# Performance work log

Measured on AMD Instinct MI355X. Metric: run time of the kernel, lower is better.

## Reference

```python
import jax, jax.numpy as jnp
import numpy as np

B, L_MAX, D, RL, RD, DOUT = 64, 4096, 128, 64, 16, 512
LN_EPS = 1e-5

def _xavier(key, shape):
    fan_in, fan_out = shape[0], shape[1]
    limit = np.sqrt(6.0 / (fan_in + fan_out)).astype(np.float32)
    return jax.random.uniform(key, shape, jnp.float32, -limit, limit)

def setup_inputs() -> dict:
    key = jax.random.key(0)
    ks = jax.random.split(key, 10)
    emb = jax.random.normal(ks[0], (B, L_MAX, D), jnp.float32)
    # contiguous padding mask from random true lengths (standard ESM padding)
    lengths = jax.random.randint(ks[1], (B,), 1, L_MAX + 1)
    mask = (jnp.arange(L_MAX)[None, :] < lengths[:, None])  # bool [B, L_max]
    B_c = _xavier(ks[2], (D, RD))
    A_c = _xavier(ks[3], (L_MAX, RL))
    H_c = _xavier(ks[4], (RL * RD, DOUT))
    W1 = _xavier(ks[5], (DOUT, DOUT))
    b1 = jnp.zeros((DOUT,), jnp.float32)
    ln_w = jnp.ones((DOUT,), jnp.float32)
    ln_b = jnp.zeros((DOUT,), jnp.float32)
    W2 = _xavier(ks[6], (DOUT, DOUT))
    b2 = jnp.zeros((DOUT,), jnp.float32)
    return {"emb": emb, "mask": mask, "B_c": B_c, "A_c": A_c, "H_c": H_c,
            "W1": W1, "b1": b1, "ln_w": ln_w, "ln_b": ln_b, "W2": W2, "b2": b2}

def reference(emb, mask, B_c, A_c, H_c, W1, b1, ln_w, ln_b, W2, b2):
    m = mask.astype(emb.dtype)                      # [B, L]
    X = emb * m[:, :, None]                         # masked embeddings [B, L, D]
    Y = jnp.einsum('bld,dr->blr', X, B_c)           # low-rank proj over D -> [B, L, rD]
    U = jnp.einsum('blr,lk->bkr', Y, A_c)           # low-rank proj over L -> [B, rL, rD]
    z = U.reshape(U.shape[0], -1) @ H_c             # [B, d]
    # expander: Linear -> LayerNorm -> ReLU -> Linear
    h = z @ W1 + b1
    mu = jnp.mean(h, axis=-1, keepdims=True)
    var = jnp.mean(jnp.square(h - mu), axis=-1, keepdims=True)
    h = (h - mu) / jnp.sqrt(var + LN_EPS) * ln_w + ln_b
    h = jax.nn.relu(h)
    return h @ W2 + b2
```

## Files before the change

kernel.cpp:

```cpp
#include <hip/hip_runtime.h>


__global__ __launch_bounds__(256) void detect_mask(
    const unsigned int* __restrict__ m, int* __restrict__ flag)
{
    unsigned int v = 0;
    int base = (blockIdx.x * 256 + threadIdx.x) * 4;
#pragma unroll
    for (int i = 0; i < 4; ++i) v |= m[base + i];
    unsigned long long any = __ballot(v > 1u);
    if ((threadIdx.x & 63) == 0 && any) atomicOr(flag, 1);
}

#define BCS_CHUNK 516
__global__ __launch_bounds__(256, 3) void y_proj(
    const float* __restrict__ emb,
    const void* __restrict__ maskp,
    const float* __restrict__ Bc,
    float* __restrict__ Y,
    const int* __restrict__ flag)
{
    __shared__ __align__(16) float BcS[4 * BCS_CHUNK];

    const int tid = threadIdx.x;
    const int q   = tid & 3;
    const int r2  = tid >> 2;
    const int b   = blockIdx.x >> 5;
    const int rg  = blockIdx.x & 31;
    const long l0 = (long)rg * 128;
    const int byte_mode = *flag;

#pragma unroll
    for (int i = 0; i < 8; ++i) {
        int e = i * 256 + tid;
        int k = e >> 4, col = e & 15;
        BcS[(k >> 5) * BCS_CHUNK + (k & 31) * 16 + col] = Bc[e];
    }
    __syncthreads();

    const long row0 = (long)b * 4096 + l0 + r2;
    const long row1 = row0 + 64;
    const float* x0p = emb + row0 * 128 + q * 32;
    const float* x1p = emb + row1 * 128 + q * 32;
    float4 xv0[8], xv1[8];
#pragma unroll
    for (int j = 0; j < 8; ++j) xv0[j] = *(const float4*)(x0p + j * 4);
#pragma unroll
    for (int j = 0; j < 8; ++j) xv1[j] = *(const float4*)(x1p + j * 4);

    const float* bq = BcS + q * BCS_CHUNK;
    float y0[16], y1[16];
#pragma unroll
    for (int j = 0; j < 16; ++j) { y0[j] = 0.f; y1[j] = 0.f; }
#pragma unroll
    for (int j4 = 0; j4 < 8; ++j4) {
        float4 v0 = xv0[j4], v1 = xv1[j4];
#pragma unroll
        for (int i = 0; i < 4; ++i) {
            int kk = j4 * 4 + i;
            float xa = (i == 0) ? v0.x : (i == 1) ? v0.y : (i == 2) ? v0.z : v0.w;
            float xb = (i == 0) ? v1.x : (i == 1) ? v1.y : (i == 2) ? v1.z : v1.w;
#pragma unroll
            for (int c4 = 0; c4 < 4; ++c4) {
                float4 bv = *(const float4*)(bq + kk * 16 + c4 * 4);
                y0[c4 * 4 + 0] += xa * bv.x; y0[c4 * 4 + 1] += xa * bv.y;
                y0[c4 * 4 + 2] += xa * bv.z; y0[c4 * 4 + 3] += xa * bv.w;
                y1[c4 * 4 + 0] += xb * bv.x; y1[c4 * 4 + 1] += xb * bv.y;
                y1[c4 * 4 + 2] += xb * bv.z; y1[c4 * 4 + 3] += xb * bv.w;
            }
        }
    }
#pragma unroll
    for (int j = 0; j < 16; ++j) {
        y0[j] += __shfl_xor(y0[j], 1); y0[j] += __shfl_xor(y0[j], 2);
        y1[j] += __shfl_xor(y1[j], 1); y1[j] += __shfl_xor(y1[j], 2);
    }

    bool mb0 = byte_mode ? (((const unsigned char*)maskp)[row0] != 0)
                         : (((const int*)maskp)[row0] != 0);
    bool mb1 = byte_mode ? (((const unsigned char*)maskp)[row1] != 0)
                         : (((const int*)maskp)[row1] != 0);
    float m0 = mb0 ? 1.f : 0.f, m1 = mb1 ? 1.f : 0.f;

    float4 o0, o1;
    if (q == 0)      { o0 = make_float4(y0[0],y0[1],y0[2],y0[3]);
                       o1 = make_float4(y1[0],y1[1],y1[2],y1[3]); }
    else if (q == 1) { o0 = make_float4(y0[4],y0[5],y0[6],y0[7]);
                       o1 = make_float4(y1[4],y1[5],y1[6],y1[7]); }
    else if (q == 2) { o0 = make_float4(y0[8],y0[9],y0[10],y0[11]);
                       o1 = make_float4(y1[8],y1[9],y1[10],y1[11]); }
    else             { o0 = make_float4(y0[12],y0[13],y0[14],y0[15]);
                       o1 = make_float4(y1[12],y1[13],y1[14],y1[15]); }
    o0.x *= m0; o0.y *= m0; o0.z *= m0; o0.w *= m0;
    o1.x *= m1; o1.y *= m1; o1.z *= m1; o1.w *= m1;
    *(float4*)(Y + row0 * 16 + q * 4) = o0;
    *(float4*)(Y + row1 * 16 + q * 4) = o1;
}

__global__ __launch_bounds__(256) void u_part(
    const float* __restrict__ Ac,
    const float* __restrict__ Y,
    float* __restrict__ Part)
{
    __shared__ __align__(16) float Lred[4 * 64 * 16];

    const int tid = threadIdx.x;
    const int cg  = tid & 3;
    const int kg  = (tid >> 2) & 15;
    const int ls  = tid >> 6;
    const int b   = blockIdx.x >> 4;
    const int c   = blockIdx.x & 15;
    const long l0 = (long)c * 256 + ls * 64;

    const float* ap = Ac + l0 * 64 + kg * 4;
    const float* yp = Y + ((long)b * 4096 + l0) * 16 + cg * 4;

    float acc[4][4];
#pragma unroll
    for (int i = 0; i < 4; ++i)
#pragma unroll
        for (int j = 0; j < 4; ++j) acc[i][j] = 0.f;

#pragma unroll 8
    for (int l = 0; l < 64; ++l) {
        float4 a4 = *(const float4*)(ap + l * 64);
        float4 y4 = *(const float4*)(yp + l * 16);
        acc[0][0] += a4.x * y4.x; acc[0][1] += a4.x * y4.y;
        acc[0][2] += a4.x * y4.z; acc[0][3] += a4.x * y4.w;
        acc[1][0] += a4.y * y4.x; acc[1][1] += a4.y * y4.y;
        acc[1][2] += a4.y * y4.z; acc[1][3] += a4.y * y4.w;
        acc[2][0] += a4.z * y4.x; acc[2][1] += a4.z * y4.y;
        acc[2][2] += a4.z * y4.z; acc[2][3] += a4.z * y4.w;
        acc[3][0] += a4.w * y4.x; acc[3][1] += a4.w * y4.y;
        acc[3][2] += a4.w * y4.z; acc[3][3] += a4.w * y4.w;
    }

#pragma unroll
    for (int i = 0; i < 4; ++i) {
        float4 p = {acc[i][0], acc[i][1], acc[i][2], acc[i][3]};
        *(float4*)(&Lred[ls * 1024 + (kg * 4 + i) * 16 + cg * 4]) = p;
    }
    __syncthreads();

    const int k  = tid >> 2;
    const int cq = tid & 3;
    float4 s0 = *(const float4*)(&Lred[0 * 1024 + k * 16 + cq * 4]);
    float4 s1 = *(const float4*)(&Lred[1 * 1024 + k * 16 + cq * 4]);
    float4 s2 = *(const float4*)(&Lred[2 * 1024 + k * 16 + cq * 4]);
    float4 s3 = *(const float4*)(&Lred[3 * 1024 + k * 16 + cq * 4]);
    float4 s;
    s.x = s0.x + s1.x + s2.x + s3.x;
    s.y = s0.y + s1.y + s2.y + s3.y;
    s.z = s0.z + s1.z + s2.z + s3.z;
    s.w = s0.w + s1.w + s2.w + s3.w;
    *(float4*)(Part + ((long)(c * 64 + b)) * 1024 + k * 16 + cq * 4) = s;
}

__global__ __launch_bounds__(256) void k2a(
    const float* __restrict__ Part,
    const float* __restrict__ Hc,
    float* __restrict__ zbuf)
{
    __shared__ __align__(16) float Us[1024];
    __shared__ __align__(16) float hp[8][128];

    const int tid = threadIdx.x;
    const int b   = blockIdx.x >> 2;
    const int jq  = blockIdx.x & 3;

    {
        const float* pb = Part + (long)b * 1024 + tid * 4;
        float4 s = {0.f, 0.f, 0.f, 0.f};
#pragma unroll
        for (int cc = 0; cc < 16; ++cc) {
            float4 v = *(const float4*)(pb + (long)cc * 64 * 1024);
            s.x += v.x; s.y += v.y; s.z += v.z; s.w += v.w;
        }
        *(float4*)(Us + tid * 4) = s;
    }
    __syncthreads();

    const int c4 = (tid & 31) * 4;
    const int kq = tid >> 5;
    const int k0 = kq * 128;
    float a0 = 0.f, a1 = 0.f, a2 = 0.f, a3 = 0.f;
    for (int k4 = 0; k4 < 128; k4 += 4) {
        float4 u = *(const float4*)(Us + k0 + k4);
        const float* hcp = Hc + (long)(k0 + k4) * 512 + jq * 128 + c4;
        float4 w0  = *(const float4*)(hcp);
        float4 w1v = *(const float4*)(hcp + 512);
        float4 w2v = *(const float4*)(hcp + 1024);
        float4 w3  = *(const float4*)(hcp + 1536);
        a0 += u.x * w0.x + u.y * w1v.x + u.z * w2v.x + u.w * w3.x;
        a1 += u.x * w0.y + u.y * w1v.y + u.z * w2v.y + u.w * w3.y;
        a2 += u.x * w0.z + u.y * w1v.z + u.z * w2v.z + u.w * w3.z;
        a3 += u.x * w0.w + u.y * w1v.w + u.z * w2v.w + u.w * w3.w;
    }
    float4 p = {a0, a1, a2, a3};
    *(float4*)(&hp[kq][c4]) = p;
    __syncthreads();

    if (tid < 128) {
        float z = hp[0][tid] + hp[1][tid] + hp[2][tid] + hp[3][tid]
                + hp[4][tid] + hp[5][tid] + hp[6][tid] + hp[7][tid];
        zbuf[(long)b * 512 + jq * 128 + tid] = z;
    }
}

__global__ __launch_bounds__(256) void k2b(
    const float* __restrict__ zbuf,
    const float* __restrict__ W1,
    const float* __restrict__ b1,
    float* __restrict__ gbuf,
    float* __restrict__ pstat)
{
    __shared__ __align__(16) float zs[512];
    __shared__ __align__(16) float hp[8][128];
    __shared__ float red[8];

    const int tid = threadIdx.x;
    const int b   = blockIdx.x >> 2;
    const int jq  = blockIdx.x & 3;

    if (tid < 128)
        *(float4*)(zs + tid * 4) = *(const float4*)(zbuf + (long)b * 512 + tid * 4);
    __syncthreads();

    const int c4 = (tid & 31) * 4;
    const int kq = tid >> 5;
    const int k0 = kq * 64;
    float a0 = 0.f, a1 = 0.f, a2 = 0.f, a3 = 0.f;
    for (int k4 = 0; k4 < 64; k4 += 4) {
        float4 u = *(const float4*)(zs + k0 + k4);
        const float* wp = W1 + (long)(k0 + k4) * 512 + jq * 128 + c4;
        float4 w0  = *(const float4*)(wp);
        float4 w1v = *(const float4*)(wp + 512);
        float4 w2v = *(const float4*)(wp + 1024);
        float4 w3  = *(const float4*)(wp + 1536);
        a0 += u.x * w0.x + u.y * w1v.x + u.z * w2v.x + u.w * w3.x;
        a1 += u.x * w0.y + u.y * w1v.y + u.z * w2v.y + u.w * w3.y;
        a2 += u.x * w0.z + u.y * w1v.z + u.z * w2v.z + u.w * w3.z;
        a3 += u.x * w0.w + u.y * w1v.w + u.z * w2v.w + u.w * w3.w;
    }
    float4 p = {a0, a1, a2, a3};
    *(float4*)(&hp[kq][c4]) = p;
    __syncthreads();

    float s = 0.f, s2 = 0.f;
    if (tid < 128) {
        float hv = hp[0][tid] + hp[1][tid] + hp[2][tid] + hp[3][tid]
                 + hp[4][tid] + hp[5][tid] + hp[6][tid] + hp[7][tid]
                 + b1[jq * 128 + tid];
        gbuf[(long)b * 512 + jq * 128 + tid] = hv;
        s = hv; s2 = hv * hv;
    }
#pragma unroll
    for (int m = 32; m >= 1; m >>= 1) {
        s  += __shfl_xor(s, m);
        s2 += __shfl_xor(s2, m);
    }
    const int wave = tid >> 6, lane = tid & 63;
    if (lane == 0) { red[wave] = s; red[wave + 4] = s2; }
    __syncthreads();
    if (tid == 0) {
        pstat[((long)b * 4 + jq) * 2 + 0] = red[0] + red[1] + red[2] + red[3];
        pstat[((long)b * 4 + jq) * 2 + 1] = red[4] + red[5] + red[6] + red[7];
    }
}

__global__ __launch_bounds__(256) void k2c(
    const float* __restrict__ gbuf,
    const float* __restrict__ pstat,
    const float* __restrict__ lnw,
    const float* __restrict__ lnb,
    const float* __restrict__ W2,
    const float* __restrict__ b2,
    float* __restrict__ out)
{
    __shared__ __align__(16) float hs[512];
    __shared__ __align__(16) float hp[8][128];

    const int tid = threadIdx.x;
    const int b   = blockIdx.x >> 2;
    const int jq  = blockIdx.x & 3;

    float S = 0.f, S2 = 0.f;
#pragma unroll
    for (int qq = 0; qq < 4; ++qq) {
        S  += pstat[((long)b * 4 + qq) * 2 + 0];
        S2 += pstat[((long)b * 4 + qq) * 2 + 1];
    }
    const float mu   = S * (1.f / 512.f);
    const float var  = S2 * (1.f / 512.f) - mu * mu;
    const float rstd = rsqrtf(var + 1e-5f);

    if (tid < 128) {
        float4 g  = *(const float4*)(gbuf + (long)b * 512 + tid * 4);
        float4 w  = *(const float4*)(lnw + tid * 4);
        float4 bb = *(const float4*)(lnb + tid * 4);
        float h0 = (g.x - mu) * rstd * w.x + bb.x;
        float h1 = (g.y - mu) * rstd * w.y + bb.y;
        float h2 = (g.z - mu) * rstd * w.z + bb.z;
        float h3 = (g.w - mu) * rstd * w.w + bb.w;
        h0 = h0 > 0.f ? h0 : 0.f;
        h1 = h1 > 0.f ? h1 : 0.f;
        h2 = h2 > 0.f ? h2 : 0.f;
        h3 = h3 > 0.f ? h3 : 0.f;
        *(float4*)(hs + tid * 4) = make_float4(h0, h1, h2, h3);
    }
    __syncthreads();

    const int c4 = (tid & 31) * 4;
    const int kq = tid >> 5;
    const int k0 = kq * 64;
    float a0 = 0.f, a1 = 0.f, a2 = 0.f, a3 = 0.f;
    for (int k4 = 0; k4 < 64; k4 += 4) {
        float4 u = *(const float4*)(hs + k0 + k4);
        const float* wp = W2 + (long)(k0 + k4) * 512 + jq * 128 + c4;
        float4 w0  = *(const float4*)(wp);
        float4 w1v = *(const float4*)(wp + 512);
        float4 w2v = *(const float4*)(wp + 1024);
        float4 w3  = *(const float4*)(wp + 1536);
        a0 += u.x * w0.x + u.y * w1v.x + u.z * w2v.x + u.w * w3.x;
        a1 += u.x * w0.y + u.y * w1v.y + u.z * w2v.y + u.w * w3.y;
        a2 += u.x * w0.z + u.y * w1v.z + u.z * w2v.z + u.w * w3.z;
        a3 += u.x * w0.w + u.y * w1v.w + u.z * w2v.w + u.w * w3.w;
    }
    float4 p = {a0, a1, a2, a3};
    *(float4*)(&hp[kq][c4]) = p;
    __syncthreads();

    if (tid < 128) {
        float o = hp[0][tid] + hp[1][tid] + hp[2][tid] + hp[3][tid]
                + hp[4][tid] + hp[5][tid] + hp[6][tid] + hp[7][tid]
                + b2[jq * 128 + tid];
        out[(long)b * 512 + jq * 128 + tid] = o;
    }
}

extern "C" void kernel_launch(void* const* d_in, const int* in_sizes, int n_in,
                              void* d_out, int out_size, void* d_ws, size_t ws_size,
                              hipStream_t stream) {
    const float* emb = (const float*)d_in[0];
    const void*  msk = (const void*)d_in[1];
    const float* Bc  = (const float*)d_in[2];
    const float* Ac  = (const float*)d_in[3];
    const float* Hc  = (const float*)d_in[4];
    const float* W1  = (const float*)d_in[5];
    const float* b1  = (const float*)d_in[6];
    const float* lnw = (const float*)d_in[7];
    const float* lnb = (const float*)d_in[8];
    const float* W2  = (const float*)d_in[9];
    const float* b2  = (const float*)d_in[10];

    float* Yw    = (float*)d_ws;
    float* Part  = Yw + (long)64 * 4096 * 16;
    int*   flg   = (int*)(Part + 16 * 64 * 1024);
    float* zbuf  = (float*)((char*)flg + 4096);
    float* gbuf  = zbuf + 64 * 512;
    float* pstat = gbuf + 64 * 512;

    hipMemsetAsync(flg, 0, 4, stream);
    detect_mask<<<64, 256, 0, stream>>>((const unsigned int*)msk, flg);
    y_proj<<<2048, 256, 0, stream>>>(emb, msk, Bc, Yw, flg);
    u_part<<<1024, 256, 0, stream>>>(Ac, Yw, Part);
    k2a<<<256, 256, 0, stream>>>(Part, Hc, zbuf);
    k2b<<<256, 256, 0, stream>>>(zbuf, W1, b1, gbuf, pstat);
    k2c<<<256, 256, 0, stream>>>(gbuf, pstat, lnw, lnb, W2, b2, (float*)d_out);
}
```

Baseline: 303.4 us.

## Fuse Y projection and L-reduction into one kernel using shared-memory Y tile

Merges the y_proj and u_part kernels so each block computes a 256-row Y tile into shared memory and immediately reduces it against A_c, removing the global Y round-trip and one launch. The emb loads are re-laid out so each thread reads interleaved float4 slices across four rows, with B_c permuted in LDS to match. This trades occupancy (more registers for 4x16 accumulators, extra LDS, the launch-bounds occupancy hint dropped) and fewer blocks for the removed global traffic.

```diff
diff --git a/kernel.cpp b/kernel.cpp
--- a/kernel.cpp
+++ b/kernel.cpp
@@ -13,107 +13,100 @@
 }
 
 #define BCS_CHUNK 516
-__global__ __launch_bounds__(256, 3) void y_proj(
+__global__ __launch_bounds__(256) void k1_fused(
     const float* __restrict__ emb,
     const void* __restrict__ maskp,
     const float* __restrict__ Bc,
-    float* __restrict__ Y,
+    const float* __restrict__ Ac,
+    float* __restrict__ Part,
     const int* __restrict__ flag)
 {
     __shared__ __align__(16) float BcS[4 * BCS_CHUNK];
+    __shared__ __align__(16) float YsL[256 * 16];
 
     const int tid = threadIdx.x;
     const int q   = tid & 3;
     const int r2  = tid >> 2;
-    const int b   = blockIdx.x >> 5;
-    const int rg  = blockIdx.x & 31;
-    const long l0 = (long)rg * 128;
+    const int b   = blockIdx.x >> 4;
+    const int c   = blockIdx.x & 15;
+    const long l0 = (long)c * 256;
     const int byte_mode = *flag;
 
 #pragma unroll
     for (int i = 0; i < 8; ++i) {
         int e = i * 256 + tid;
         int k = e >> 4, col = e & 15;
-        BcS[(k >> 5) * BCS_CHUNK + (k & 31) * 16 + col] = Bc[e];
-    }
-    __syncthreads();
-
-    const long row0 = (long)b * 4096 + l0 + r2;
-    const long row1 = row0 + 64;
-    const float* x0p = emb + row0 * 128 + q * 32;
-    const float* x1p = emb + row1 * 128 + q * 32;
-    float4 xv0[8], xv1[8];
-#pragma unroll
-    for (int j = 0; j < 8; ++j) xv0[j] = *(const float4*)(x0p + j * 4);
-#pragma unroll
-    for (int j = 0; j < 8; ++j) xv1[j] = *(const float4*)(x1p + j * 4);
+        int qk = (k >> 2) & 3;
+        int loc = ((k >> 4) << 2) | (k & 3);
+        BcS[qk * BCS_CHUNK + loc * 16 + col] = Bc[e];
+    }
+    __syncthreads();
+
+    float y[4][16];
+#pragma unroll
+    for (int m = 0; m < 4; ++m)
+#pragma unroll
+        for (int j = 0; j < 16; ++j) y[m][j] = 0.f;
 
     const float* bq = BcS + q * BCS_CHUNK;
-    float y0[16], y1[16];
-#pragma unroll
-    for (int j = 0; j < 16; ++j) { y0[j] = 0.f; y1[j] = 0.f; }
+    const float* xb = emb + ((long)b * 4096 + l0 + r2) * 128 + q * 4;
+
 #pragma unroll
     for (int j4 = 0; j4 < 8; ++j4) {
-        float4 v0 = xv0[j4], v1 = xv1[j4];
+        float4 xr[4];
+#pragma unroll
+        for (int m = 0; m < 4; ++m)
+            xr[m] = *(const float4*)(xb + (long)m * 64 * 128 + j4 * 16);
 #pragma unroll
         for (int i = 0; i < 4; ++i) {
-            int kk = j4 * 4 + i;
-            float xa = (i == 0) ? v0.x : (i == 1) ? v0.y : (i == 2) ? v0.z : v0.w;
-            float xb = (i == 0) ? v1.x : (i == 1) ? v1.y : (i == 2) ? v1.z : v1.w;
+            float x0 = (i == 0) ? xr[0].x : (i == 1) ? xr[0].y : (i == 2) ? xr[0].z : xr[0].w;
+            float x1 = (i == 0) ? xr[1].x : (i == 1) ? xr[1].y : (i == 2) ? xr[1].z : xr[1].w;
+            float x2 = (i == 0) ? xr[2].x : (i == 1) ? xr[2].y : (i == 2) ? xr[2].z : xr[2].w;
+            float x3 = (i == 0) ? xr[3].x : (i == 1) ? xr[3].y : (i == 2) ? xr[3].z : xr[3].w;
 #pragma unroll
             for (int c4 = 0; c4 < 4; ++c4) {
-                float4 bv = *(const float4*)(bq + kk * 16 + c4 * 4);
-                y0[c4 * 4 + 0] += xa * bv.x; y0[c4 * 4 + 1] += xa * bv.y;
-                y0[c4 * 4 + 2] += xa * bv.z; y0[c4 * 4 + 3] += xa * bv.w;
-                y1[c4 * 4 + 0] += xb * bv.x; y1[c4 * 4 + 1] += xb * bv.y;
-                y1[c4 * 4 + 2] += xb * bv.z; y1[c4 * 4 + 3] += xb * bv.w;
+                float4 bv = *(const float4*)(bq + (j4 * 4 + i) * 16 + c4 * 4);
+                y[0][c4 * 4 + 0] += x0 * bv.x; y[0][c4 * 4 + 1] += x0 * bv.y;
+                y[0][c4 * 4 + 2] += x0 * bv.z; y[0][c4 * 4 + 3] += x0 * bv.w;
+                y[1][c4 * 4 + 0] += x1 * bv.x; y[1][c4 * 4 + 1] += x1 * bv.y;
+                y[1][c4 * 4 + 2] += x1 * bv.z; y[1][c4 * 4 + 3] += x1 * bv.w;
+                y[2][c4 * 4 + 0] += x2 * bv.x; y[2][c4 * 4 + 1] += x2 * bv.y;
+                y[2][c4 * 4 + 2] += x2 * bv.z; y[2][c4 * 4 + 3] += x2 * bv.w;
+                y[3][c4 * 4 + 0] += x3 * bv.x; y[3][c4 * 4 + 1] += x3 * bv.y;
+                y[3][c4 * 4 + 2] += x3 * bv.z; y[3][c4 * 4 + 3] += x3 * bv.w;
             }
         }
     }
-#pragma unroll
-    for (int j = 0; j < 16; ++j) {
-        y0[j] += __shfl_xor(y0[j], 1); y0[j] += __shfl_xor(y0[j], 2);
-        y1[j] += __shfl_xor(y1[j], 1); y1[j] += __shfl_xor(y1[j], 2);
-    }
-
-    bool mb0 = byte_mode ? (((const unsigned char*)maskp)[row0] != 0)
-                         : (((const int*)maskp)[row0] != 0);
-    bool mb1 = byte_mode ? (((const unsigned char*)maskp)[row1] != 0)
-                         : (((const int*)maskp)[row1] != 0);
-    float m0 = mb0 ? 1.f : 0.f, m1 = mb1 ? 1.f : 0.f;
-
-    float4 o0, o1;
-    if (q == 0)      { o0 = make_float4(y0[0],y0[1],y0[2],y0[3]);
-                       o1 = make_float4(y1[0],y1[1],y1[2],y1[3]); }
-    else if (q == 1) { o0 = make_float4(y0[4],y0[5],y0[6],y0[7]);
-                       o1 = make_float4(y1[4],y1[5],y1[6],y1[7]); }
-    else if (q == 2) { o0 = make_float4(y0[8],y0[9],y0[10],y0[11]);
-                       o1 = make_float4(y1[8],y1[9],y1[10],y1[11]); }
-    else             { o0 = make_float4(y0[12],y0[13],y0[14],y0[15]);
-                       o1 = make_float4(y1[12],y1[13],y1[14],y1[15]); }
-    o0.x *= m0; o0.y *= m0; o0.z *= m0; o0.w *= m0;
-    o1.x *= m1; o1.y *= m1; o1.z *= m1; o1.w *= m1;
-    *(float4*)(Y + row0 * 16 + q * 4) = o0;
-    *(float4*)(Y + row1 * 16 + q * 4) = o1;
-}
-
-__global__ __launch_bounds__(256) void u_part(
-    const float* __restrict__ Ac,
-    const float* __restrict__ Y,
-    float* __restrict__ Part)
-{
-    __shared__ __align__(16) float Lred[4 * 64 * 16];
-
-    const int tid = threadIdx.x;
-    const int cg  = tid & 3;
-    const int kg  = (tid >> 2) & 15;
-    const int ls  = tid >> 6;
-    const int b   = blockIdx.x >> 4;
-    const int c   = blockIdx.x & 15;
-    const long l0 = (long)c * 256 + ls * 64;
-
-    const float* ap = Ac + l0 * 64 + kg * 4;
-    const float* yp = Y + ((long)b * 4096 + l0) * 16 + cg * 4;
+
+#pragma unroll
+    for (int m = 0; m < 4; ++m)
+#pragma unroll
+        for (int j = 0; j < 16; ++j) {
+            y[m][j] += __shfl_xor(y[m][j], 1);
+            y[m][j] += __shfl_xor(y[m][j], 2);
+        }
+
+#pragma unroll
+    for (int m = 0; m < 4; ++m) {
+        long midx = (long)b * 4096 + l0 + r2 + m * 64;
+        bool mb = byte_mode ? (((const unsigned char*)maskp)[midx] != 0)
+                            : (((const int*)maskp)[midx] != 0);
+        float mv = mb ? 1.f : 0.f;
+        float4 o;
+        if (q == 0)      o = make_float4(y[m][0],  y[m][1],  y[m][2],  y[m][3]);
+        else if (q == 1) o = make_float4(y[m][4],  y[m][5],  y[m][6],  y[m][7]);
+        else if (q == 2) o = make_float4(y[m][8],  y[m][9],  y[m][10], y[m][11]);
+        else             o = make_float4(y[m][12], y[m][13], y[m][14], y[m][15]);
+        o.x *= mv; o.y *= mv; o.z *= mv; o.w *= mv;
+        *(float4*)(YsL + (r2 + m * 64) * 16 + q * 4) = o;
+    }
+    __syncthreads();
+
+    const int cg = tid & 3;
+    const int kg = (tid >> 2) & 15;
+    const int ls = tid >> 6;
+    const float* ap = Ac + (l0 + ls * 64) * 64 + kg * 4;
+    const float* yl = YsL + (ls * 64) * 16 + cg * 4;
 
     float acc[4][4];
 #pragma unroll
@@ -124,7 +117,7 @@
 #pragma unroll 8
     for (int l = 0; l < 64; ++l) {
         float4 a4 = *(const float4*)(ap + l * 64);
-        float4 y4 = *(const float4*)(yp + l * 16);
+        float4 y4 = *(const float4*)(yl + l * 16);
         acc[0][0] += a4.x * y4.x; acc[0][1] += a4.x * y4.y;
         acc[0][2] += a4.x * y4.z; acc[0][3] += a4.x * y4.w;
         acc[1][0] += a4.y * y4.x; acc[1][1] += a4.y * y4.y;
@@ -134,7 +127,9 @@
         acc[3][0] += a4.w * y4.x; acc[3][1] += a4.w * y4.y;
         acc[3][2] += a4.w * y4.z; acc[3][3] += a4.w * y4.w;
     }
-
+    __syncthreads();
+
+    float* Lred = YsL;
 #pragma unroll
     for (int i = 0; i < 4; ++i) {
         float4 p = {acc[i][0], acc[i][1], acc[i][2], acc[i][3]};
@@ -353,17 +348,15 @@
     const float* W2  = (const float*)d_in[9];
     const float* b2  = (const float*)d_in[10];
 
-    float* Yw    = (float*)d_ws;
-    float* Part  = Yw + (long)64 * 4096 * 16;
-    int*   flg   = (int*)(Part + 16 * 64 * 1024);
+    float* Part  = (float*)d_ws;
+    int*   flg   = (int*)((char*)d_ws + 4 * 1024 * 1024);
     float* zbuf  = (float*)((char*)flg + 4096);
     float* gbuf  = zbuf + 64 * 512;
     float* pstat = gbuf + 64 * 512;
 
     hipMemsetAsync(flg, 0, 4, stream);
     detect_mask<<<64, 256, 0, stream>>>((const unsigned int*)msk, flg);
-    y_proj<<<2048, 256, 0, stream>>>(emb, msk, Bc, Yw, flg);
-    u_part<<<1024, 256, 0, stream>>>(Ac, Yw, Part);
+    k1_fused<<<1024, 256, 0, stream>>>(emb, msk, Bc, Ac, Part, flg);
     k2a<<<256, 256, 0, stream>>>(Part, Hc, zbuf);
     k2b<<<256, 256, 0, stream>>>(zbuf, W1, b1, gbuf, pstat);
     k2c<<<256, 256, 0, stream>>>(gbuf, pstat, lnw, lnb, W2, b2, (float*)d_out);
```

Result: faster. 258.7 us (-14.7%).
